# Optimization experiments

Measured on AMD Instinct MI355X. Metric: run time of the kernel, lower is better.

Reference implementation:

```python
import jax, jax.numpy as jnp
import numpy as np

NF4 = jnp.array([-1.0, -0.6961928009986877, -0.5250730514526367, -0.39491748809814453,
                 -0.28444138169288635, -0.18477343022823334, -0.09105003625154495, 0.0,
                 0.07958029955625534, 0.16093020141124725, 0.24611230850219726,
                 0.33791524171829224, 0.44070982933044434, 0.5626170039176941,
                 0.7229568362236023, 1.0], dtype=jnp.float32)

OUT, IN = 8192, 8192
BLOCK = 64
NUMEL = OUT * IN


def setup_inputs() -> dict:
    key = jax.random.key(0)
    k1, k2, k3, k4 = jax.random.split(key, 4)
    x = jax.random.normal(k1, (64, IN), dtype=jnp.float32)
    packed = jax.random.randint(k2, (NUMEL // 2,), 0, 256, dtype=jnp.int32)
    absmax = jax.random.uniform(k3, (NUMEL // BLOCK,), dtype=jnp.float32)
    bias = jax.random.normal(k4, (OUT,), dtype=jnp.float32)
    return {"x": x, "packed": packed, "absmax": absmax, "bias": bias}


def nf4_dequantize(packed, absmax):
    # packed holds two 4-bit codes per byte: low nibble first, then high nibble
    low = packed & 15
    high = (packed >> 4) & 15
    q = jnp.stack([low, high], axis=1).reshape(-1)          # [numel]
    normalized = NF4[q]                                      # LUT dequant
    groups = normalized.reshape(-1, BLOCK)                   # [numel/block, block]
    w = (groups * absmax[:, None]).reshape(-1)[:NUMEL]
    return w.reshape(OUT, IN)


def reference(x, packed, absmax, bias):
    w = nf4_dequantize(packed, absmax)                       # [out, in]
    return jnp.dot(x, w.T) + bias                            # F.linear
```

## Files before the change

kernel.cpp:

```cpp
#include <hip/hip_runtime.h>
#include <hip/hip_bf16.h>

#define OUT_N 8192
#define IN_K  8192
#define M_ROWS 64

typedef __attribute__((ext_vector_type(8))) short  bf16x8;
typedef __attribute__((ext_vector_type(4))) float  f32x4;
typedef __attribute__((ext_vector_type(4))) int    int4v;

__device__ const float NF4_TAB[16] = {
  -1.0f, -0.6961928009986877f, -0.5250730514526367f, -0.39491748809814453f,
  -0.28444138169288635f, -0.18477343022823334f, -0.09105003625154495f, 0.0f,
  0.07958029955625534f, 0.16093020141124725f, 0.24611230850219726f,
  0.33791524171829224f, 0.44070982933044434f, 0.5626170039176941f,
  0.7229568362236023f, 1.0f };

static __device__ __forceinline__ unsigned short f2bf(float f) {
  union { __hip_bfloat16 h; unsigned short s; } u;
  u.h = __float2bfloat16(f);
  return u.s;
}

static __device__ __forceinline__ void gload_lds16(const void* g, void* s) {
  __builtin_amdgcn_global_load_lds((const __attribute__((address_space(1))) void*)g,
                                   (__attribute__((address_space(3))) void*)s,
                                   16, 0, 0);
}

__global__ __launch_bounds__(256) void qlin_prep(const float* __restrict__ x,
                                                 unsigned short* __restrict__ xf) {
  int t = blockIdx.x * 256 + threadIdx.x;
  int lane = t & 63, mt = (t >> 6) & 3, ks = t >> 8;
  int ri = lane & 15, kbb = lane >> 4;
  const float* src = x + (size_t)(mt * 16 + ri) * IN_K + ks * 32 + kbb * 8;
  f32x4 a = *(const f32x4*)src;
  f32x4 c = *(const f32x4*)(src + 4);
  bf16x8 o;
  o[0] = (short)f2bf(a[0]); o[1] = (short)f2bf(a[1]);
  o[2] = (short)f2bf(a[2]); o[3] = (short)f2bf(a[3]);
  o[4] = (short)f2bf(c[0]); o[5] = (short)f2bf(c[1]);
  o[6] = (short)f2bf(c[2]); o[7] = (short)f2bf(c[3]);
  ((bf16x8*)xf)[t] = o;
}

static __device__ __forceinline__ bf16x8 deq(const unsigned int* lut, int4v cur) {
  int4v bw;
  bw[0] = (int)lut[cur[0] & 255];
  bw[1] = (int)lut[cur[1] & 255];
  bw[2] = (int)lut[cur[2] & 255];
  bw[3] = (int)lut[cur[3] & 255];
  union { int4v i; bf16x8 h; } c; c.i = bw;
  return c.h;
}

#define STAGE(BUF, PH) {                                                      \
    const char* _s = xfb + (((size_t)(PH) * 4 + w) * 4096) + l * 16;          \
    gload_lds16(_s,        &ast[BUF][w][0]);                                  \
    gload_lds16(_s + 1024, &ast[BUF][w][64]);                                 \
    gload_lds16(_s + 2048, &ast[BUF][w][128]);                                \
    gload_lds16(_s + 3072, &ast[BUF][w][192]); }

#define CSTEP_BODY(S, PKV)                                                    \
    int _nk = KS + (S) + 4; if (_nk > NITm1) _nk = NITm1;                     \
    int4v _npk = *(const int4v*)(pcoal + (size_t)_nk * 64);                   \
    bf16x8 A0 = ast[cur][S][l];                                               \
    bf16x8 A1 = ast[cur][S][64 + l];                                          \
    bf16x8 A2 = ast[cur][S][128 + l];                                         \
    bf16x8 A3 = ast[cur][S][192 + l];                                         \
    int4v _c;                                                                 \
    _c[0] = __builtin_amdgcn_ds_bpermute(bpidx, PKV[0]);                      \
    _c[1] = __builtin_amdgcn_ds_bpermute(bpidx, PKV[1]);                      \
    _c[2] = __builtin_amdgcn_ds_bpermute(bpidx, PKV[2]);                      \
    _c[3] = __builtin_amdgcn_ds_bpermute(bpidx, PKV[3]);                      \
    bf16x8 b = deq(lut, _c);

#define CSTEP_EVEN(S, PKV) {                                                  \
    CSTEP_BODY(S, PKV)                                                        \
    sb0 = __builtin_amdgcn_mfma_f32_16x16x32_bf16(A0, b, zro, 0, 0, 0);       \
    sb1 = __builtin_amdgcn_mfma_f32_16x16x32_bf16(A1, b, zro, 0, 0, 0);       \
    sb2 = __builtin_amdgcn_mfma_f32_16x16x32_bf16(A2, b, zro, 0, 0, 0);       \
    sb3 = __builtin_amdgcn_mfma_f32_16x16x32_bf16(A3, b, zro, 0, 0, 0);       \
    PKV = _npk; }

#define CSTEP_ODD(S, PKV, AM) {                                               \
    CSTEP_BODY(S, PKV)                                                        \
    sb0 = __builtin_amdgcn_mfma_f32_16x16x32_bf16(A0, b, sb0, 0, 0, 0);       \
    sb1 = __builtin_amdgcn_mfma_f32_16x16x32_bf16(A1, b, sb1, 0, 0, 0);       \
    sb2 = __builtin_amdgcn_mfma_f32_16x16x32_bf16(A2, b, sb2, 0, 0, 0);       \
    sb3 = __builtin_amdgcn_mfma_f32_16x16x32_bf16(A3, b, sb3, 0, 0, 0);       \
    mn0 += sb0 * (AM); mn1 += sb1 * (AM);                                     \
    mn2 += sb2 * (AM); mn3 += sb3 * (AM);                                     \
    PKV = _npk; }

template<int NC>
__global__ __launch_bounds__(256, 4) void qlin_main(
    const int*   __restrict__ packed,
    const float* __restrict__ absmax,
    const unsigned short* __restrict__ xf,
    float*       __restrict__ parts) {
  constexpr int KCn   = IN_K / NC;
  constexpr int NIT   = KCn / 32;
  constexpr int NITm1 = NIT - 1;
  constexpr int NPH   = NIT / 4;
  constexpr int AMX   = NIT / 2 - 1;
  constexpr int LOG   = (NC == 8) ? 3 : 2;

  __shared__ unsigned int lut[256];
  __shared__ bf16x8 ast[2][4][256];
  {
    int t = threadIdx.x;
    unsigned lo = f2bf(NF4_TAB[t & 15]);
    unsigned hi = f2bf(NF4_TAB[(t >> 4) & 15]);
    lut[t] = lo | (hi << 16);
  }
  __syncthreads();

  const int l     = threadIdx.x & 63;
  const int w     = threadIdx.x >> 6;
  const int ntile = (int)blockIdx.x >> LOG;
  const int chunk = (int)blockIdx.x & (NC - 1);
  const int colg0 = ntile * 64 + w * 16;
  const int col   = colg0 + (l & 15);
  const int kb    = l >> 4;
  const int kc0   = chunk * KCn;
  const int ksg0  = kc0 >> 5;

  const char* pcoal = (const char*)packed
                    + ((size_t)(colg0 + (l >> 2)) * (IN_K / 2) + kc0 / 2) * 4
                    + (l & 3) * 16;
  const int bpidx = (((l & 15) << 2) | (l >> 4)) << 2;

  const char* xfb = (const char*)xf + (size_t)ksg0 * 4096;
  const float* aptr = absmax + (size_t)col * 128 + (kc0 >> 6);

  const f32x4 zro = {0.f, 0.f, 0.f, 0.f};
  f32x4 mn0 = zro, mn1 = zro, mn2 = zro, mn3 = zro;
  f32x4 sb0, sb1, sb2, sb3;
  int4v pk0, pk1, pk2, pk3;

  float amE = aptr[0], amO = aptr[1];
  STAGE(0, 0);
  __builtin_amdgcn_sched_barrier(0);
  pk0 = *(const int4v*)(pcoal);
  pk1 = *(const int4v*)(pcoal + 64);
  pk2 = *(const int4v*)(pcoal + 128);
  pk3 = *(const int4v*)(pcoal + 192);
  asm volatile("s_waitcnt vmcnt(4)" ::: "memory");
  __builtin_amdgcn_s_barrier();

  for (int ph = 0; ph < NPH; ++ph) {
    const int KS  = ph * 4;
    const int cur = ph & 1;

    int ia = 2 * ph + 2; if (ia > AMX) ia = AMX;
    int ib = 2 * ph + 3; if (ib > AMX) ib = AMX;
    float pmE = aptr[ia], pmO = aptr[ib];
    if (ph + 1 < NPH) STAGE(cur ^ 1, ph + 1);
    __builtin_amdgcn_sched_barrier(0);

    CSTEP_EVEN(0, pk0)
    CSTEP_ODD (1, pk1, amE)
    CSTEP_EVEN(2, pk2)
    CSTEP_ODD (3, pk3, amO)

    amE = pmE; amO = pmO;
    asm volatile("s_waitcnt vmcnt(4)" ::: "memory");
    asm volatile("s_waitcnt lgkmcnt(0)" ::: "memory");
    __builtin_amdgcn_s_barrier();
  }

  float* po = parts + (size_t)chunk * M_ROWS * OUT_N + col;
  const int rbase = kb * 4;
  po[(size_t)(0  + rbase + 0) * OUT_N] = mn0[0];
  po[(size_t)(0  + rbase + 1) * OUT_N] = mn0[1];
  po[(size_t)(0  + rbase + 2) * OUT_N] = mn0[2];
  po[(size_t)(0  + rbase + 3) * OUT_N] = mn0[3];
  po[(size_t)(16 + rbase + 0) * OUT_N] = mn1[0];
  po[(size_t)(16 + rbase + 1) * OUT_N] = mn1[1];
  po[(size_t)(16 + rbase + 2) * OUT_N] = mn1[2];
  po[(size_t)(16 + rbase + 3) * OUT_N] = mn1[3];
  po[(size_t)(32 + rbase + 0) * OUT_N] = mn2[0];
  po[(size_t)(32 + rbase + 1) * OUT_N] = mn2[1];
  po[(size_t)(32 + rbase + 2) * OUT_N] = mn2[2];
  po[(size_t)(32 + rbase + 3) * OUT_N] = mn2[3];
  po[(size_t)(48 + rbase + 0) * OUT_N] = mn3[0];
  po[(size_t)(48 + rbase + 1) * OUT_N] = mn3[1];
  po[(size_t)(48 + rbase + 2) * OUT_N] = mn3[2];
  po[(size_t)(48 + rbase + 3) * OUT_N] = mn3[3];
}

template<int NC>
__global__ __launch_bounds__(256) void qlin_reduce(
    const float* __restrict__ parts,
    const float* __restrict__ bias,
    float*       __restrict__ out) {
  const int TOT4 = M_ROWS * OUT_N / 4;
  int i4 = blockIdx.x * 256 + threadIdx.x;
  if (i4 >= TOT4) return;
  const f32x4* p = (const f32x4*)parts;
  f32x4 s = p[i4];
  #pragma unroll
  for (int c = 1; c < NC; ++c) s += p[i4 + c * TOT4];
  f32x4 bb = ((const f32x4*)bias)[i4 & (OUT_N / 4 - 1)];
  ((f32x4*)out)[i4] = s + bb;
}

extern "C" void kernel_launch(void* const* d_in, const int* in_sizes, int n_in,
                              void* d_out, int out_size, void* d_ws, size_t ws_size,
                              hipStream_t stream) {
  const float* x      = (const float*)d_in[0];
  const int*   packed = (const int*)d_in[1];
  const float* absmax = (const float*)d_in[2];
  const float* bias   = (const float*)d_in[3];
  float* out = (float*)d_out;

  unsigned short* xf = (unsigned short*)d_ws;
  float* parts = (float*)((char*)d_ws + (1 << 20));

  qlin_prep<<<(M_ROWS * IN_K / 8 + 255) / 256, 256, 0, stream>>>(x, xf);

  const size_t need8 = (size_t)(1 << 20)
                     + (size_t)8 * M_ROWS * OUT_N * sizeof(float);
  if (ws_size >= need8) {
    qlin_main<8><<<(OUT_N / 64) * 8, 256, 0, stream>>>(packed, absmax, xf, parts);
    qlin_reduce<8><<<(M_ROWS * OUT_N / 4 + 255) / 256, 256, 0, stream>>>(parts, bias, out);
  } else {
    qlin_main<4><<<(OUT_N / 64) * 4, 256, 0, stream>>>(packed, absmax, xf, parts);
    qlin_reduce<4><<<(M_ROWS * OUT_N / 4 + 255) / 256, 256, 0, stream>>>(parts, bias, out);
  }
}
```

Measured before the change: 40.98 us.

## Deepen packed-weight prefetch to eight steps and store split-K partials as bf16

The main loop now keeps eight packed-weight registers in flight instead of four. It unrolls two phases per iteration so each phase uses its own register set, which hides more global-load latency. Split-K partial sums are written as bf16 instead of fp32, halving partial-buffer write and read traffic, and the reduce kernel is rewritten to read 8 bf16 values per thread. This raises register pressure and loses precision in the partial sums, which may hurt accuracy. The vmcnt(4) wait inside the phase is left unchanged, so it may no longer match the deeper queue.

```diff
diff --git a/kernel.cpp b/kernel.cpp
--- a/kernel.cpp
+++ b/kernel.cpp
@@ -62,7 +62,7 @@
     gload_lds16(_s + 3072, &ast[BUF][w][192]); }
 
 #define CSTEP_BODY(S, PKV)                                                    \
-    int _nk = KS + (S) + 4; if (_nk > NITm1) _nk = NITm1;                     \
+    int _nk = KS + (S) + 8; if (_nk > NITm1) _nk = NITm1;                     \
     int4v _npk = *(const int4v*)(pcoal + (size_t)_nk * 64);                   \
     bf16x8 A0 = ast[cur][S][l];                                               \
     bf16x8 A1 = ast[cur][S][64 + l];                                          \
@@ -93,12 +93,29 @@
     mn2 += sb2 * (AM); mn3 += sb3 * (AM);                                     \
     PKV = _npk; }
 
+#define PHASE(PH, P0, P1, P2, P3) {                                          \
+    const int KS  = (PH) * 4;                                                \
+    const int cur = (PH) & 1;                                                \
+    int ia = 2 * (PH) + 2; if (ia > AMX) ia = AMX;                           \
+    int ib = 2 * (PH) + 3; if (ib > AMX) ib = AMX;                           \
+    float pmE = aptr[ia], pmO = aptr[ib];                                    \
+    if ((PH) + 1 < NPH) STAGE(cur ^ 1, (PH) + 1);                            \
+    __builtin_amdgcn_sched_barrier(0);                                       \
+    CSTEP_EVEN(0, P0)                                                        \
+    CSTEP_ODD (1, P1, amE)                                                   \
+    CSTEP_EVEN(2, P2)                                                        \
+    CSTEP_ODD (3, P3, amO)                                                   \
+    amE = pmE; amO = pmO;                                                    \
+    asm volatile("s_waitcnt vmcnt(4)" ::: "memory");                         \
+    asm volatile("s_waitcnt lgkmcnt(0)" ::: "memory");                       \
+    __builtin_amdgcn_s_barrier(); }
+
 template<int NC>
 __global__ __launch_bounds__(256, 4) void qlin_main(
     const int*   __restrict__ packed,
     const float* __restrict__ absmax,
     const unsigned short* __restrict__ xf,
-    float*       __restrict__ parts) {
+    unsigned short* __restrict__ parts) {
   constexpr int KCn   = IN_K / NC;
   constexpr int NIT   = KCn / 32;
   constexpr int NITm1 = NIT - 1;
@@ -137,7 +154,7 @@
   const f32x4 zro = {0.f, 0.f, 0.f, 0.f};
   f32x4 mn0 = zro, mn1 = zro, mn2 = zro, mn3 = zro;
   f32x4 sb0, sb1, sb2, sb3;
-  int4v pk0, pk1, pk2, pk3;
+  int4v pk0, pk1, pk2, pk3, pk4, pk5, pk6, pk7;
 
   float amE = aptr[0], amO = aptr[1];
   STAGE(0, 0);
@@ -146,64 +163,65 @@
   pk1 = *(const int4v*)(pcoal + 64);
   pk2 = *(const int4v*)(pcoal + 128);
   pk3 = *(const int4v*)(pcoal + 192);
-  asm volatile("s_waitcnt vmcnt(4)" ::: "memory");
+  pk4 = *(const int4v*)(pcoal + 256);
+  pk5 = *(const int4v*)(pcoal + 320);
+  pk6 = *(const int4v*)(pcoal + 384);
+  pk7 = *(const int4v*)(pcoal + 448);
+  asm volatile("s_waitcnt vmcnt(8)" ::: "memory");
   __builtin_amdgcn_s_barrier();
 
-  for (int ph = 0; ph < NPH; ++ph) {
-    const int KS  = ph * 4;
-    const int cur = ph & 1;
-
-    int ia = 2 * ph + 2; if (ia > AMX) ia = AMX;
-    int ib = 2 * ph + 3; if (ib > AMX) ib = AMX;
-    float pmE = aptr[ia], pmO = aptr[ib];
-    if (ph + 1 < NPH) STAGE(cur ^ 1, ph + 1);
-    __builtin_amdgcn_sched_barrier(0);
-
-    CSTEP_EVEN(0, pk0)
-    CSTEP_ODD (1, pk1, amE)
-    CSTEP_EVEN(2, pk2)
-    CSTEP_ODD (3, pk3, amO)
-
-    amE = pmE; amO = pmO;
-    asm volatile("s_waitcnt vmcnt(4)" ::: "memory");
-    asm volatile("s_waitcnt lgkmcnt(0)" ::: "memory");
-    __builtin_amdgcn_s_barrier();
-  }
-
-  float* po = parts + (size_t)chunk * M_ROWS * OUT_N + col;
+  for (int ph = 0; ph < NPH; ph += 2) {
+    PHASE(ph,     pk0, pk1, pk2, pk3)
+    PHASE(ph + 1, pk4, pk5, pk6, pk7)
+  }
+
+  unsigned short* po = parts + (size_t)chunk * M_ROWS * OUT_N + col;
   const int rbase = kb * 4;
-  po[(size_t)(0  + rbase + 0) * OUT_N] = mn0[0];
-  po[(size_t)(0  + rbase + 1) * OUT_N] = mn0[1];
-  po[(size_t)(0  + rbase + 2) * OUT_N] = mn0[2];
-  po[(size_t)(0  + rbase + 3) * OUT_N] = mn0[3];
-  po[(size_t)(16 + rbase + 0) * OUT_N] = mn1[0];
-  po[(size_t)(16 + rbase + 1) * OUT_N] = mn1[1];
-  po[(size_t)(16 + rbase + 2) * OUT_N] = mn1[2];
-  po[(size_t)(16 + rbase + 3) * OUT_N] = mn1[3];
-  po[(size_t)(32 + rbase + 0) * OUT_N] = mn2[0];
-  po[(size_t)(32 + rbase + 1) * OUT_N] = mn2[1];
-  po[(size_t)(32 + rbase + 2) * OUT_N] = mn2[2];
-  po[(size_t)(32 + rbase + 3) * OUT_N] = mn2[3];
-  po[(size_t)(48 + rbase + 0) * OUT_N] = mn3[0];
-  po[(size_t)(48 + rbase + 1) * OUT_N] = mn3[1];
-  po[(size_t)(48 + rbase + 2) * OUT_N] = mn3[2];
-  po[(size_t)(48 + rbase + 3) * OUT_N] = mn3[3];
+  po[(size_t)(0  + rbase + 0) * OUT_N] = f2bf(mn0[0]);
+  po[(size_t)(0  + rbase + 1) * OUT_N] = f2bf(mn0[1]);
+  po[(size_t)(0  + rbase + 2) * OUT_N] = f2bf(mn0[2]);
+  po[(size_t)(0  + rbase + 3) * OUT_N] = f2bf(mn0[3]);
+  po[(size_t)(16 + rbase + 0) * OUT_N] = f2bf(mn1[0]);
+  po[(size_t)(16 + rbase + 1) * OUT_N] = f2bf(mn1[1]);
+  po[(size_t)(16 + rbase + 2) * OUT_N] = f2bf(mn1[2]);
+  po[(size_t)(16 + rbase + 3) * OUT_N] = f2bf(mn1[3]);
+  po[(size_t)(32 + rbase + 0) * OUT_N] = f2bf(mn2[0]);
+  po[(size_t)(32 + rbase + 1) * OUT_N] = f2bf(mn2[1]);
+  po[(size_t)(32 + rbase + 2) * OUT_N] = f2bf(mn2[2]);
+  po[(size_t)(32 + rbase + 3) * OUT_N] = f2bf(mn2[3]);
+  po[(size_t)(48 + rbase + 0) * OUT_N] = f2bf(mn3[0]);
+  po[(size_t)(48 + rbase + 1) * OUT_N] = f2bf(mn3[1]);
+  po[(size_t)(48 + rbase + 2) * OUT_N] = f2bf(mn3[2]);
+  po[(size_t)(48 + rbase + 3) * OUT_N] = f2bf(mn3[3]);
 }
 
 template<int NC>
 __global__ __launch_bounds__(256) void qlin_reduce(
-    const float* __restrict__ parts,
+    const unsigned short* __restrict__ parts,
     const float* __restrict__ bias,
     float*       __restrict__ out) {
-  const int TOT4 = M_ROWS * OUT_N / 4;
-  int i4 = blockIdx.x * 256 + threadIdx.x;
-  if (i4 >= TOT4) return;
-  const f32x4* p = (const f32x4*)parts;
-  f32x4 s = p[i4];
+  int t = blockIdx.x * 256 + threadIdx.x;
+  if (t >= M_ROWS * OUT_N / 8) return;
+  const size_t off = (size_t)t * 8;
+  float s[8] = {0,0,0,0,0,0,0,0};
   #pragma unroll
-  for (int c = 1; c < NC; ++c) s += p[i4 + c * TOT4];
-  f32x4 bb = ((const f32x4*)bias)[i4 & (OUT_N / 4 - 1)];
-  ((f32x4*)out)[i4] = s + bb;
+  for (int c = 0; c < NC; ++c) {
+    bf16x8 v = *(const bf16x8*)(parts + (size_t)c * M_ROWS * OUT_N + off);
+    #pragma unroll
+    for (int j = 0; j < 8; ++j)
+      s[j] += __uint_as_float(((unsigned)(unsigned short)v[j]) << 16);
+  }
+  const int colb = t & (OUT_N / 8 - 1);
+  const f32x4* bp = (const f32x4*)(bias + colb * 8);
+  f32x4 b0 = bp[0], b1 = bp[1];
+  f32x4 o0, o1;
+  o0[0] = s[0] + b0[0]; o0[1] = s[1] + b0[1];
+  o0[2] = s[2] + b0[2]; o0[3] = s[3] + b0[3];
+  o1[0] = s[4] + b1[0]; o1[1] = s[5] + b1[1];
+  o1[2] = s[6] + b1[2]; o1[3] = s[7] + b1[3];
+  float* op = out + off;
+  *(f32x4*)op = o0;
+  *(f32x4*)(op + 4) = o1;
 }
 
 extern "C" void kernel_launch(void* const* d_in, const int* in_sizes, int n_in,
@@ -215,18 +233,18 @@
   const float* bias   = (const float*)d_in[3];
   float* out = (float*)d_out;
 
-  unsigned short* xf = (unsigned short*)d_ws;
-  float* parts = (float*)((char*)d_ws + (1 << 20));
+  unsigned short* xf    = (unsigned short*)d_ws;
+  unsigned short* parts = (unsigned short*)((char*)d_ws + (1 << 20));
 
   qlin_prep<<<(M_ROWS * IN_K / 8 + 255) / 256, 256, 0, stream>>>(x, xf);
 
   const size_t need8 = (size_t)(1 << 20)
-                     + (size_t)8 * M_ROWS * OUT_N * sizeof(float);
+                     + (size_t)8 * M_ROWS * OUT_N * sizeof(unsigned short);
   if (ws_size >= need8) {
     qlin_main<8><<<(OUT_N / 64) * 8, 256, 0, stream>>>(packed, absmax, xf, parts);
-    qlin_reduce<8><<<(M_ROWS * OUT_N / 4 + 255) / 256, 256, 0, stream>>>(parts, bias, out);
+    qlin_reduce<8><<<(M_ROWS * OUT_N / 8 + 255) / 256, 256, 0, stream>>>(parts, bias, out);
   } else {
     qlin_main<4><<<(OUT_N / 64) * 4, 256, 0, stream>>>(packed, absmax, xf, parts);
-    qlin_reduce<4><<<(M_ROWS * OUT_N / 4 + 255) / 256, 256, 0, stream>>>(parts, bias, out);
-  }
-}
+    qlin_reduce<4><<<(M_ROWS * OUT_N / 8 + 255) / 256, 256, 0, stream>>>(parts, bias, out);
+  }
+}
```

New measurement: 97.78 us. +138.6%, slower.
